# Kernel optimization log

Measured on AMD Instinct MI355X. Metric: run time of the kernel, lower is better.

The kernel has to match this reference:

```python
import jax, jax.numpy as jnp
import numpy as np

IN_FEATURES = 1024
BATCH = 65536


def setup_inputs() -> dict:
    key = jax.random.key(0)
    ks = jax.random.split(key, 7)
    return {
        "x": jax.random.normal(ks[0], (BATCH, IN_FEATURES), dtype=jnp.float32),
        "W": jax.random.normal(ks[1], (IN_FEATURES, IN_FEATURES), dtype=jnp.float32),
        "P": jax.random.normal(ks[2], (IN_FEATURES,), dtype=jnp.float32),
        "w": jax.random.normal(ks[3], (1,), dtype=jnp.float32),
        "p": jax.random.normal(ks[4], (1,), dtype=jnp.float32),
        "sine_w": jax.random.normal(ks[5], (1,), dtype=jnp.float32),
        "cosine_w": jax.random.normal(ks[6], (1,), dtype=jnp.float32),
    }


def reference(x, W, P, w, p, sine_w, cosine_w):
    # Time2Vec: linear term + periodic (sin/cos mixed) term, concatenated.
    original = w * x + p                      # [B, F]
    z = jnp.matmul(x, W) + P                  # [B, F]
    periodic = sine_w * jnp.sin(z) + cosine_w * jnp.cos(z)  # [B, F]
    return jnp.concatenate((original, periodic), axis=-1)    # [B, 2F]
```

## Files before the change

### kernel.cpp

```cpp
#include <hip/hip_runtime.h>


typedef __attribute__((ext_vector_type(4))) float    f32x4;
typedef __attribute__((ext_vector_type(8))) short    short8;
typedef __attribute__((ext_vector_type(4))) unsigned short u16x4;

#define IN_F   1024
#define BATCH  65536
#define BM     128
#define BN     128
#define BK     32

__device__ __forceinline__ unsigned short f2bf(float f) {
    unsigned u = __float_as_uint(f);
    u += 0x7fffu + ((u >> 16) & 1u);
    return (unsigned short)(u >> 16);
}
__device__ __forceinline__ float bf2f(unsigned short b) {
    return __uint_as_float(((unsigned)b) << 16);
}

__device__ __forceinline__ void async_copy16(const void* g, void* l) {
    __builtin_amdgcn_global_load_lds(
        (const __attribute__((address_space(1))) void*)g,
        (__attribute__((address_space(3))) void*)l, 16, 0, 0);
}

__global__ __launch_bounds__(256) void prep_x_kernel(
    const f32x4* __restrict__ x4, const float* __restrict__ wp,
    const float* __restrict__ pp, float* __restrict__ out,
    u16x4* __restrict__ Xhi, u16x4* __restrict__ Xlo)
{
    unsigned idx = blockIdx.x * 256u + threadIdx.x;
    f32x4 v = x4[idx];
    float w = wp[0], p = pp[0];
    unsigned e = idx * 4u;
    unsigned r = e >> 10, cc = e & 1023u;
    f32x4 o = v * w + p;
    *(f32x4*)(out + (size_t)r * 2048 + cc) = o;
    u16x4 h, l;
#pragma unroll
    for (int i = 0; i < 4; ++i) {
        unsigned short hh = f2bf(v[i]);
        h[i] = hh;
        l[i] = f2bf(v[i] - bf2f(hh));
    }
    Xhi[idx] = h;
    Xlo[idx] = l;
}

__global__ __launch_bounds__(256) void prep_w_kernel(
    const float* __restrict__ W,
    unsigned short* __restrict__ Whi, unsigned short* __restrict__ Wlo)
{
    __shared__ float t[32][33];
    int tx = threadIdx.x, ty = threadIdx.y;
    int n0 = blockIdx.x * 32, k0 = blockIdx.y * 32;
#pragma unroll
    for (int i = 0; i < 4; ++i)
        t[ty + i * 8][tx] = W[(size_t)(k0 + ty + i * 8) * IN_F + n0 + tx];
    __syncthreads();
#pragma unroll
    for (int i = 0; i < 4; ++i) {
        float v = t[tx][ty + i * 8];
        int n = n0 + ty + i * 8, k = k0 + tx;
        unsigned short h = f2bf(v);
        Whi[(size_t)n * IN_F + k] = h;
        Wlo[(size_t)n * IN_F + k] = f2bf(v - bf2f(h));
    }
}

__global__ __launch_bounds__(256, 2) void gemm_kernel(
    const unsigned short* __restrict__ Xhi, const unsigned short* __restrict__ Xlo,
    const unsigned short* __restrict__ Whi, const unsigned short* __restrict__ Wlo,
    const float* __restrict__ P, const float* __restrict__ swp,
    const float* __restrict__ cwp, float* __restrict__ out)
{
    __shared__ unsigned short As[BM * BK];
    __shared__ unsigned short Bs[BN * BK];

    const int tid  = threadIdx.x;
    const int lane = tid & 63;
    const int wave = tid >> 6;

    int bid = blockIdx.x;
    int c = bid & 7, s = bid >> 3;
    int m_blk = (s >> 3) * 8 + c;
    int n_blk = s & 7;
    const int m0 = m_blk * BM;
    const int n0 = n_blk * BN;

    const int srow = lane >> 2;
    const int scol = (lane & 3) * 8;

    const int fr = lane & 15;
    const int fk = (lane >> 4) * 8;
    const int wm = wave & 1;
    const int wn = wave >> 1;

    f32x4 acc[4][4] = {};

    for (int kt = 0; kt < 96; ++kt) {
        const int part = kt >> 5;
        const int k0   = (kt & 31) * BK;
        const unsigned short* Ap = (part == 2) ? Xlo : Xhi;
        const unsigned short* Bp = (part == 1) ? Wlo : Whi;

        __syncthreads();
#pragma unroll
        for (int cc = 0; cc < 2; ++cc) {
            int chunk = wave * 2 + cc;
            const unsigned short* ga =
                Ap + (size_t)(m0 + chunk * 16 + srow) * IN_F + k0 + scol;
            async_copy16(ga, (char*)As + chunk * 1024 + lane * 16);
            const unsigned short* gb =
                Bp + (size_t)(n0 + chunk * 16 + srow) * IN_F + k0 + scol;
            async_copy16(gb, (char*)Bs + chunk * 1024 + lane * 16);
        }
        __syncthreads();

        short8 a[4], b[4];
#pragma unroll
        for (int i = 0; i < 4; ++i) {
            a[i] = *(const short8*)&As[(wm * 64 + i * 16 + fr) * BK + fk];
            b[i] = *(const short8*)&Bs[(wn * 64 + i * 16 + fr) * BK + fk];
        }
#pragma unroll
        for (int i = 0; i < 4; ++i)
#pragma unroll
            for (int j = 0; j < 4; ++j)
                acc[i][j] = __builtin_amdgcn_mfma_f32_16x16x32_bf16(
                    a[i], b[j], acc[i][j], 0, 0, 0);
    }

    const float sw = swp[0], cw = cwp[0];
#pragma unroll
    for (int j = 0; j < 4; ++j) {
        const int colg = n0 + wn * 64 + j * 16 + (lane & 15);
        const float pcol = P[colg];
#pragma unroll
        for (int i = 0; i < 4; ++i) {
#pragma unroll
            for (int r = 0; r < 4; ++r) {
                int rowg = m0 + wm * 64 + i * 16 + (lane >> 4) * 4 + r;
                float z = acc[i][j][r] + pcol;
                float val = sw * __sinf(z) + cw * __cosf(z);
                out[(size_t)rowg * 2048 + 1024 + colg] = val;
            }
        }
    }
}

__global__ __launch_bounds__(256) void naive_kernel(
    const float* __restrict__ x, const float* __restrict__ W,
    const float* __restrict__ P, const float* __restrict__ wp,
    const float* __restrict__ pp, const float* __restrict__ swp,
    const float* __restrict__ cwp, float* __restrict__ out)
{
    size_t idx = (size_t)blockIdx.x * 256 + threadIdx.x;
    if (idx >= (size_t)BATCH * IN_F) return;
    size_t r = idx >> 10;
    int n = (int)(idx & 1023);
    float acc = 0.f;
    for (int k = 0; k < IN_F; ++k)
        acc = fmaf(x[r * IN_F + k], W[(size_t)k * IN_F + n], acc);
    float z = acc + P[n];
    out[r * 2048 + n] = wp[0] * x[r * IN_F + n] + pp[0];
    out[r * 2048 + 1024 + n] = swp[0] * __sinf(z) + cwp[0] * __cosf(z);
}

extern "C" void kernel_launch(void* const* d_in, const int* in_sizes, int n_in,
                              void* d_out, int out_size, void* d_ws, size_t ws_size,
                              hipStream_t stream)
{
    const float* x   = (const float*)d_in[0];
    const float* W   = (const float*)d_in[1];
    const float* P   = (const float*)d_in[2];
    const float* w   = (const float*)d_in[3];
    const float* p   = (const float*)d_in[4];
    const float* swv = (const float*)d_in[5];
    const float* cwv = (const float*)d_in[6];
    float* out = (float*)d_out;

    const size_t xElems = (size_t)BATCH * IN_F;
    const size_t wElems = (size_t)IN_F * IN_F;
    const size_t need   = xElems * 2 * 2 + wElems * 2 * 2;

    if (ws_size >= need) {
        unsigned short* Xhi = (unsigned short*)d_ws;
        unsigned short* Xlo = Xhi + xElems;
        unsigned short* Whi = Xlo + xElems;
        unsigned short* Wlo = Whi + wElems;

        prep_x_kernel<<<65536, 256, 0, stream>>>(
            (const f32x4*)x, w, p, out, (u16x4*)Xhi, (u16x4*)Xlo);
        prep_w_kernel<<<dim3(32, 32), dim3(32, 8), 0, stream>>>(W, Whi, Wlo);
        gemm_kernel<<<4096, 256, 0, stream>>>(Xhi, Xlo, Whi, Wlo, P, swv, cwv, out);
    } else {
        naive_kernel<<<(unsigned)((xElems + 255) / 256), 256, 0, stream>>>(
            x, W, P, w, p, swv, cwv, out);
    }
}
```

Baseline: 1.180 ms.

## Restructure GEMM to 256x256 tiles with 4-stage async LDS pipeline

Replaces the 128x128, 256-thread GEMM with a 256x256 tile per 512-thread block. It uses a 4-deep ring of LDS buffers filled by async global-to-LDS loads issued three k-steps ahead, an XOR-swizzled LDS layout to avoid bank conflicts, and a split A-load schedule with s_setprio around the MFMA bursts. The aim is to raise data reuse per loaded byte and hide global-load latency behind matrix math, which the old load-sync-compute loop could not do. In exchange it uses 128 KB of LDS per block, which likely limits occupancy to one block per CU, and it relies on hand-tuned vmcnt waits and barriers that must be exactly right.

```diff
diff --git a/kernel.cpp b/kernel.cpp
--- a/kernel.cpp
+++ b/kernel.cpp
@@ -7,9 +7,6 @@
 
 #define IN_F   1024
 #define BATCH  65536
-#define BM     128
-#define BN     128
-#define BK     32
 
 __device__ __forceinline__ unsigned short f2bf(float f) {
     unsigned u = __float_as_uint(f);
@@ -70,79 +67,111 @@
     }
 }
 
-__global__ __launch_bounds__(256, 2) void gemm_kernel(
+__global__ __launch_bounds__(512, 2) void gemm_kernel(
     const unsigned short* __restrict__ Xhi, const unsigned short* __restrict__ Xlo,
     const unsigned short* __restrict__ Whi, const unsigned short* __restrict__ Wlo,
     const float* __restrict__ P, const float* __restrict__ swp,
     const float* __restrict__ cwp, float* __restrict__ out)
 {
-    __shared__ unsigned short As[BM * BK];
-    __shared__ unsigned short Bs[BN * BK];
+    __shared__ __align__(16) char As[65536];
+    __shared__ __align__(16) char Bs[65536];
 
     const int tid  = threadIdx.x;
     const int lane = tid & 63;
     const int wave = tid >> 6;
+    const int wm   = wave >> 2;
+    const int wn   = wave & 3;
 
     int bid = blockIdx.x;
-    int c = bid & 7, s = bid >> 3;
-    int m_blk = (s >> 3) * 8 + c;
-    int n_blk = s & 7;
-    const int m0 = m_blk * BM;
-    const int n0 = n_blk * BN;
-
-    const int srow = lane >> 2;
-    const int scol = (lane & 3) * 8;
-
-    const int fr = lane & 15;
-    const int fk = (lane >> 4) * 8;
-    const int wm = wave & 1;
-    const int wn = wave >> 1;
-
-    f32x4 acc[4][4] = {};
-
-    for (int kt = 0; kt < 96; ++kt) {
-        const int part = kt >> 5;
-        const int k0   = (kt & 31) * BK;
-        const unsigned short* Ap = (part == 2) ? Xlo : Xhi;
-        const unsigned short* Bp = (part == 1) ? Wlo : Whi;
-
-        __syncthreads();
-#pragma unroll
-        for (int cc = 0; cc < 2; ++cc) {
-            int chunk = wave * 2 + cc;
-            const unsigned short* ga =
-                Ap + (size_t)(m0 + chunk * 16 + srow) * IN_F + k0 + scol;
-            async_copy16(ga, (char*)As + chunk * 1024 + lane * 16);
-            const unsigned short* gb =
-                Bp + (size_t)(n0 + chunk * 16 + srow) * IN_F + k0 + scol;
-            async_copy16(gb, (char*)Bs + chunk * 1024 + lane * 16);
-        }
-        __syncthreads();
-
-        short8 a[4], b[4];
-#pragma unroll
-        for (int i = 0; i < 4; ++i) {
-            a[i] = *(const short8*)&As[(wm * 64 + i * 16 + fr) * BK + fk];
-            b[i] = *(const short8*)&Bs[(wn * 64 + i * 16 + fr) * BK + fk];
-        }
+    int wg  = (bid & 7) * 128 + (bid >> 3);
+    const int m0 = (wg >> 2) * 256;
+    const int n0 = (wg & 3) * 256;
+
+    const int fr    = lane & 15;
+    const int fsw   = (fr ^ (fr >> 2)) & 3;
+    const int slotp = (lane >> 4) ^ fsw;
+    const unsigned aoff = (unsigned)((wm * 128 + fr) * 64 + slotp * 16);
+    const unsigned boff = (unsigned)((wn * 64 + fr) * 64 + slotp * 16);
+
+    const int srow  = tid >> 2;
+    const int sslot = (tid & 3) ^ (((tid >> 2) ^ (tid >> 4)) & 3);
+    const size_t aRow0 = (size_t)(m0 + srow) * IN_F + sslot * 8;
+    const size_t aRow1 = (size_t)(m0 + 128 + srow) * IN_F + sslot * 8;
+    const size_t bRow0 = (size_t)(n0 + srow) * IN_F + sslot * 8;
+    const size_t bRow1 = (size_t)(n0 + 128 + srow) * IN_F + sslot * 8;
+    const unsigned ldsW = (unsigned)(wave * 1024);
+
+    f32x4 acc[8][4] = {};
+
+    auto stageA = [&](int kt) {
+        const unsigned short* Ap = ((kt >> 5) == 2) ? Xlo : Xhi;
+        int k0e = (kt & 31) * 32;
+        char* d = As + (kt & 3) * 16384 + ldsW;
+        async_copy16(Ap + aRow0 + k0e, d);
+        async_copy16(Ap + aRow1 + k0e, d + 8192);
+    };
+    auto stageB = [&](int kt) {
+        const unsigned short* Bp = ((kt >> 5) == 1) ? Wlo : Whi;
+        int k0e = (kt & 31) * 32;
+        char* d = Bs + (kt & 3) * 16384 + ldsW;
+        async_copy16(Bp + bRow0 + k0e, d);
+        async_copy16(Bp + bRow1 + k0e, d + 8192);
+    };
+
+    stageA(0); stageB(0);
+    stageA(1); stageB(1);
+    stageA(2); stageB(2);
+    asm volatile("s_waitcnt vmcnt(8)" ::: "memory");
+    __builtin_amdgcn_s_barrier();
+
+    for (int t = 0; t < 96; ++t) {
+        const char* aBase = As + (t & 3) * 16384 + aoff;
+        const char* bBase = Bs + (t & 3) * 16384 + boff;
+        short8 av[4], bv[4], av2[4];
+
+#pragma unroll
+        for (int i = 0; i < 4; ++i) av[i] = *(const short8*)(aBase + i * 1024);
+#pragma unroll
+        for (int j = 0; j < 4; ++j) bv[j] = *(const short8*)(bBase + j * 1024);
+        if (t + 3 < 96) stageA(t + 3);
+        __builtin_amdgcn_s_barrier();
+        __builtin_amdgcn_s_setprio(1);
 #pragma unroll
         for (int i = 0; i < 4; ++i)
 #pragma unroll
             for (int j = 0; j < 4; ++j)
                 acc[i][j] = __builtin_amdgcn_mfma_f32_16x16x32_bf16(
-                    a[i], b[j], acc[i][j], 0, 0, 0);
+                    av[i], bv[j], acc[i][j], 0, 0, 0);
+        __builtin_amdgcn_s_setprio(0);
+        __builtin_amdgcn_s_barrier();
+
+#pragma unroll
+        for (int i = 0; i < 4; ++i) av2[i] = *(const short8*)(aBase + 4096 + i * 1024);
+        if (t + 3 < 96) stageB(t + 3);
+        __builtin_amdgcn_s_barrier();
+        __builtin_amdgcn_s_setprio(1);
+#pragma unroll
+        for (int i = 0; i < 4; ++i)
+#pragma unroll
+            for (int j = 0; j < 4; ++j)
+                acc[4 + i][j] = __builtin_amdgcn_mfma_f32_16x16x32_bf16(
+                    av2[i], bv[j], acc[4 + i][j], 0, 0, 0);
+        __builtin_amdgcn_s_setprio(0);
+        if (t < 93) { asm volatile("s_waitcnt vmcnt(8)" ::: "memory"); }
+        else        { asm volatile("s_waitcnt vmcnt(0)" ::: "memory"); }
+        __builtin_amdgcn_s_barrier();
     }
 
     const float sw = swp[0], cw = cwp[0];
 #pragma unroll
     for (int j = 0; j < 4; ++j) {
-        const int colg = n0 + wn * 64 + j * 16 + (lane & 15);
+        const int colg = n0 + wn * 64 + j * 16 + fr;
         const float pcol = P[colg];
 #pragma unroll
-        for (int i = 0; i < 4; ++i) {
+        for (int i = 0; i < 8; ++i) {
 #pragma unroll
             for (int r = 0; r < 4; ++r) {
-                int rowg = m0 + wm * 64 + i * 16 + (lane >> 4) * 4 + r;
+                int rowg = m0 + wm * 128 + i * 16 + (lane >> 4) * 4 + r;
                 float z = acc[i][j][r] + pcol;
                 float val = sw * __sinf(z) + cw * __cosf(z);
                 out[(size_t)rowg * 2048 + 1024 + colg] = val;
@@ -195,7 +224,7 @@
         prep_x_kernel<<<65536, 256, 0, stream>>>(
             (const f32x4*)x, w, p, out, (u16x4*)Xhi, (u16x4*)Xlo);
         prep_w_kernel<<<dim3(32, 32), dim3(32, 8), 0, stream>>>(W, Whi, Wlo);
-        gemm_kernel<<<4096, 256, 0, stream>>>(Xhi, Xlo, Whi, Wlo, P, swv, cwv, out);
+        gemm_kernel<<<1024, 512, 0, stream>>>(Xhi, Xlo, Whi, Wlo, P, swv, cwv, out);
     } else {
         naive_kernel<<<(unsigned)((xElems + 255) / 256), 256, 0, stream>>>(
             x, W, P, w, p, swv, cwv, out);
```

Measured after the change: 1.161 ms. No clear change (-1.6%).
